# Optimization experiments

Hardware: AMD Instinct MI355X
Metric: run time of the kernel (lower is better)

Reference implementation:

```python
import jax, jax.numpy as jnp
import numpy as np

B, NQ, NK, C, H = 4, 1024, 1024, 768, 12
DH = C // H
SCALE = DH ** -0.5
EPS = 1e-5  # nn.LayerNorm default
NEG_INF = float('-inf')


def _ln(x, g, b):
    m = jnp.mean(x, axis=-1, keepdims=True)
    v = jnp.mean((x - m) ** 2, axis=-1, keepdims=True)
    return (x - m) * jax.lax.rsqrt(v + EPS) * g + b


def _heads(t):  # [B,N,C] -> [B,H,N,Dh]
    Bq, N, _ = t.shape
    return t.reshape(Bq, N, H, DH).transpose(0, 2, 1, 3)


def setup_inputs() -> dict:
    key = jax.random.key(0)
    ks = jax.random.split(key, 32)
    w = lambda k, shape: jax.random.normal(k, shape, jnp.float32) * 0.02
    g = lambda k: 1.0 + jax.random.normal(k, (C,), jnp.float32) * 0.02
    b = lambda k: jax.random.normal(k, (C,), jnp.float32) * 0.02
    inp = {
        'x': jax.random.normal(ks[0], (B, NQ, C), jnp.float32),
        'y': jax.random.normal(ks[1], (B, NK, C), jnp.float32),
        'xpos': jnp.arange(B * NQ, dtype=jnp.int32).reshape(B, NQ),
        'ypos': jnp.arange(B * NK, dtype=jnp.int32).reshape(B, NK),
        'mask': jax.random.randint(ks[2], (NQ, NK), 0, 2) > 0,
        'similarities': jax.random.normal(ks[3], (B, H, NQ, NK), jnp.float32),
        # norms
        'ln1_g': g(ks[4]), 'ln1_b': b(ks[5]),
        'ln2_g': g(ks[6]), 'ln2_b': b(ks[7]),
        'ln3_g': g(ks[8]), 'ln3_b': b(ks[9]),
        'lny_g': g(ks[10]), 'lny_b': b(ks[11]),
        # self-attn (qkv_bias=False)
        'qkv_w': w(ks[12], (3 * C, C)),
        'aproj_w': w(ks[13], (C, C)), 'aproj_b': b(ks[14]),
        # cross-attn
        'pq_w': w(ks[15], (C, C)), 'pk_w': w(ks[16], (C, C)), 'pv_w': w(ks[17], (C, C)),
        'cproj_w': w(ks[18], (C, C)), 'cproj_b': b(ks[19]),
        # mlp (hidden = 4*C)
        'fc1_w': w(ks[20], (4 * C, C)), 'fc1_b': jax.random.normal(ks[21], (4 * C,), jnp.float32) * 0.02,
        'fc2_w': w(ks[22], (C, 4 * C)), 'fc2_b': b(ks[23]),
    }
    return inp


def reference(x, y, xpos, ypos, mask, similarities,
              ln1_g, ln1_b, ln2_g, ln2_b, ln3_g, ln3_b, lny_g, lny_b,
              qkv_w, aproj_w, aproj_b,
              pq_w, pk_w, pv_w, cproj_w, cproj_b,
              fc1_w, fc1_b, fc2_w, fc2_b):
    # ---- self-attention (rope=None, dropout=0) ----
    xn = _ln(x, ln1_g, ln1_b)
    qkv = (xn @ qkv_w.T).reshape(B, NQ, 3, H, DH).transpose(2, 0, 3, 1, 4)
    q, k, v = qkv[0], qkv[1], qkv[2]                       # [B,H,Nq,Dh]
    attn = jax.nn.softmax(jnp.einsum('bhqd,bhkd->bhqk', q, k) * SCALE, axis=-1)
    sa = jnp.einsum('bhqk,bhkd->bhqd', attn, v).transpose(0, 2, 1, 3).reshape(B, NQ, C)
    x = x + sa @ aproj_w.T + aproj_b

    # ---- sparse cross-attention with similarity bias + mask ----
    y_ = _ln(y, lny_g, lny_b)
    xn2 = _ln(x, ln2_g, ln2_b)
    cq = _heads(xn2 @ pq_w.T)                              # [B,H,Nq,Dh]
    ck = _heads(y_ @ pk_w.T)                               # [B,H,Nk,Dh]
    cv = _heads(y_ @ pv_w.T)
    scores = jnp.einsum('bhqd,bhkd->bhqk', cq, ck) * SCALE
    sims_c = similarities - jnp.mean(similarities, axis=1, keepdims=True)
    scores = scores + sims_c
    scores = jnp.where(mask[None, None], scores, NEG_INF)
    cattn = jax.nn.softmax(scores, axis=-1)
    ca = jnp.einsum('bhqk,bhkd->bhqd', cattn, cv).transpose(0, 2, 1, 3).reshape(B, NQ, C)
    x = x + ca @ cproj_w.T + cproj_b

    # ---- MLP (exact GELU, as nn.GELU default) ----
    xn3 = _ln(x, ln3_g, ln3_b)
    h = jax.nn.gelu(xn3 @ fc1_w.T + fc1_b, approximate=False)
    x = x + h @ fc2_w.T + fc2_b
    return (x, y)
```

## Files before the change

kernel.cpp:

```cpp
#include <hip/hip_runtime.h>
#include <cstdint>
#include <cstddef>


typedef __bf16 bf16;
typedef __attribute__((ext_vector_type(8))) __bf16 bf16x8;
typedef __attribute__((ext_vector_type(4))) __bf16 bf16x4;
typedef __attribute__((ext_vector_type(4))) float f32x4;

typedef __attribute__((address_space(1))) void gvoid;
typedef __attribute__((address_space(3))) void lvoid;

#define DEVI static __device__ __forceinline__

DEVI void gload16(const void* g, void* l) {
  __builtin_amdgcn_global_load_lds((gvoid*)(uintptr_t)g, (lvoid*)(uintptr_t)l, 16, 0, 0);
}

DEVI f32x4 mfma_bf16(bf16x8 a, bf16x8 b, f32x4 c) {
  return __builtin_amdgcn_mfma_f32_16x16x32_bf16(a, b, c, 0, 0, 0);
}


template<int BM, int BN, bool BIAS, bool GELU, bool RES, bool OBF, bool VT>
DEVI void gemm_dev(bf16* As, bf16* Bs, int by, int bx,
                   const bf16* __restrict__ A, const bf16* __restrict__ Bt,
                   const float* __restrict__ bias, const float* __restrict__ res,
                   bf16* __restrict__ Cb, float* __restrict__ Cf,
                   bf16* __restrict__ vtOut, int vtBase, int N, int K)
{
  constexpr int WM = BM / 2, WN = BN / 2;
  constexpr int FM = WM / 16, FN = WN / 16;
  const int tid = threadIdx.x;
  const int lane = tid & 63;
  const int wv = tid >> 6;
  const int wr = wv >> 1, wc = wv & 1;
  const int l15 = lane & 15, lg = lane >> 4;
  const int bm = by * BM, bn = bx * BN;

  f32x4 acc[FM][FN];
  const f32x4 z = {0.f, 0.f, 0.f, 0.f};
  #pragma unroll
  for (int i = 0; i < FM; ++i)
    #pragma unroll
    for (int jj = 0; jj < FN; ++jj) acc[i][jj] = z;

  for (int k0 = 0; k0 < K; k0 += 64) {
    __syncthreads();
    #pragma unroll
    for (int c = tid; c < BM * 8; c += 256) {
      const int row = c >> 3, colb = (c & 7) << 4;
      gload16((const char*)A + ((size_t)(bm + row) * K + k0) * 2 + colb,
              (char*)As + (size_t)c * 16);
    }
    #pragma unroll
    for (int c = tid; c < BN * 8; c += 256) {
      const int row = c >> 3, colb = (c & 7) << 4;
      gload16((const char*)Bt + ((size_t)(bn + row) * K + k0) * 2 + colb,
              (char*)Bs + (size_t)c * 16);
    }
    __syncthreads();
    #pragma unroll
    for (int kk = 0; kk < 64; kk += 32) {
      bf16x8 af[FM], bfr[FN];
      #pragma unroll
      for (int mi = 0; mi < FM; ++mi)
        af[mi] = *(const bf16x8*)(As + (size_t)(wr * WM + mi * 16 + l15) * 64 + kk + lg * 8);
      #pragma unroll
      for (int ni = 0; ni < FN; ++ni)
        bfr[ni] = *(const bf16x8*)(Bs + (size_t)(wc * WN + ni * 16 + l15) * 64 + kk + lg * 8);
      #pragma unroll
      for (int mi = 0; mi < FM; ++mi)
        #pragma unroll
        for (int ni = 0; ni < FN; ++ni)
          acc[mi][ni] = mfma_bf16(af[mi], bfr[ni], acc[mi][ni]);
    }
  }

  #pragma unroll
  for (int mi = 0; mi < FM; ++mi) {
    const int row0 = bm + wr * WM + mi * 16 + lg * 4;
    #pragma unroll
    for (int ni = 0; ni < FN; ++ni) {
      const int col = bn + wc * WN + ni * 16 + l15;
      if constexpr (VT) {
        if (col >= vtBase) {
          const int hd = col - vtBase;
          const int bb = row0 >> 10, n0 = row0 & 1023;
          bf16x4 ov;
          #pragma unroll
          for (int r = 0; r < 4; ++r) ov[r] = (bf16)acc[mi][ni][r];
          *(bf16x4*)(vtOut + ((size_t)(bb * 768 + hd)) * 1024 + n0) = ov;
          continue;
        }
      }
      #pragma unroll
      for (int r = 0; r < 4; ++r) {
        float v = acc[mi][ni][r];
        if constexpr (BIAS) v += bias[col];
        if constexpr (GELU) v = 0.5f * v * (1.0f + erff(v * 0.70710678118654752f));
        if constexpr (RES)  v += res[(size_t)(row0 + r) * N + col];
        if constexpr (OBF)  Cb[(size_t)(row0 + r) * N + col] = (bf16)v;
        else                Cf[(size_t)(row0 + r) * N + col] = v;
      }
    }
  }
}

DEVI void biasr_dev(int blk,
                    const float* __restrict__ sim,
                    const unsigned char* __restrict__ mask,
                    bf16* __restrict__ out)
{
  const int b = blk >> 10, q = blk & 1023;
  const int t = threadIdx.x, lane = t & 63;

  int ds = 0;
  #pragma unroll
  for (int i = 0; i < 4; ++i) {
    const int idx = (lane * 4 + i) * 4;
    ds += mask[idx + 1] + mask[idx + 2] + mask[idx + 3];
  }
  #pragma unroll
  for (int o = 32; o; o >>= 1) ds += __shfl_xor(ds, o);
  const int msh = (ds == 0) ? 2 : 0;

  const int k4 = t * 4;
  const float* sb = sim + (size_t)b * 12 * 1048576;
  f32x4 sv[12];
  f32x4 acc = {0.f, 0.f, 0.f, 0.f};
  #pragma unroll
  for (int h = 0; h < 12; ++h) {
    sv[h] = *(const f32x4*)(sb + ((size_t)h * 1024 + q) * 1024 + k4);
    acc += sv[h];
  }
  const f32x4 mean = acc * (1.0f / 12.0f);

  float mb[4];
  if (msh == 0) {
    const uchar4 mv = *(const uchar4*)(mask + (size_t)q * 1024 + k4);
    mb[0] = mv.x ? 0.f : -1e30f; mb[1] = mv.y ? 0.f : -1e30f;
    mb[2] = mv.z ? 0.f : -1e30f; mb[3] = mv.w ? 0.f : -1e30f;
  } else {
    const int4 mv = *(const int4*)((const int*)mask + (size_t)q * 1024 + k4);
    mb[0] = mv.x ? 0.f : -1e30f; mb[1] = mv.y ? 0.f : -1e30f;
    mb[2] = mv.z ? 0.f : -1e30f; mb[3] = mv.w ? 0.f : -1e30f;
  }

  bf16* ob = out + (size_t)(b * 1024 + q) * 12 * 1024;
  #pragma unroll
  for (int h = 0; h < 12; ++h) {
    bf16x4 o;
    #pragma unroll
    for (int j = 0; j < 4; ++j)
      o[j] = (bf16)(sv[h][j] - mean[j] + mb[j]);
    *(bf16x4*)(ob + h * 1024 + k4) = o;
  }
}

DEVI void lnw_dev(int row,
                  const float* __restrict__ xin, const float* __restrict__ g,
                  const float* __restrict__ be, bf16* __restrict__ out)
{
  const int lane = threadIdx.x & 63;
  const f32x4* xr = (const f32x4*)(xin + (size_t)row * 768);
  f32x4 v[3];
  #pragma unroll
  for (int j = 0; j < 3; ++j) v[j] = xr[lane + 64 * j];
  float s = 0.f;
  #pragma unroll
  for (int j = 0; j < 3; ++j) s += v[j][0] + v[j][1] + v[j][2] + v[j][3];
  #pragma unroll
  for (int o = 32; o; o >>= 1) s += __shfl_xor(s, o);
  const float mean = s * (1.0f / 768.0f);
  float q = 0.f;
  #pragma unroll
  for (int j = 0; j < 3; ++j)
    #pragma unroll
    for (int e = 0; e < 4; ++e) { const float d = v[j][e] - mean; q += d * d; }
  #pragma unroll
  for (int o = 32; o; o >>= 1) q += __shfl_xor(q, o);
  const float inv = rsqrtf(q * (1.0f / 768.0f) + 1e-5f);
  #pragma unroll
  for (int j = 0; j < 3; ++j) {
    const int c = lane + 64 * j;
    const f32x4 gv = ((const f32x4*)g)[c];
    const f32x4 bv = ((const f32x4*)be)[c];
    bf16x4 o4;
    #pragma unroll
    for (int e = 0; e < 4; ++e)
      o4[e] = (bf16)((v[j][e] - mean) * inv * gv[e] + bv[e]);
    *((bf16x4*)out + (size_t)row * 192 + c) = o4;
  }
}

struct AuxArgs {
  const float* csrc[7];
  bf16* cdst[7];
  int cend[7];
  const float* y; const float* gy; const float* byv; bf16* yln;
  const float* sim; const unsigned char* mask; bf16* biasOut;
  int biasStart, biasCount, extraStart, extraCount;
};

DEVI void aux_dev(int j, const AuxArgs& A)
{
  if (j < A.extraCount) {
    const int e = A.extraStart + j;
    if (e < 1024) {
      lnw_dev(e * 4 + (threadIdx.x >> 6), A.y, A.gy, A.byv, A.yln);
    } else {
      const int blk = e - 1024;
      const int t = threadIdx.x;
      #pragma unroll
      for (int u = 0; u < 4; ++u) {
        const int i = blk * 1024 + u * 256 + t;
        int s = 0;
        #pragma unroll
        for (int k = 0; k < 6; ++k) s += (i >= A.cend[k]) ? 1 : 0;
        const int base = s ? A.cend[s - 1] : 0;
        const int off = i - base;
        const f32x4 v = *((const f32x4*)A.csrc[s] + off);
        bf16x4 o;
        o[0] = (bf16)v[0]; o[1] = (bf16)v[1]; o[2] = (bf16)v[2]; o[3] = (bf16)v[3];
        *(bf16x4*)(A.cdst[s] + (size_t)off * 4) = o;
      }
    }
  } else {
    biasr_dev(A.biasStart + (j - A.extraCount), A.sim, A.mask, A.biasOut);
  }
}


__global__ __launch_bounds__(256)
void prep_k(const float* __restrict__ qkvw, bf16* __restrict__ w_qkv,
            const float* __restrict__ x, const float* __restrict__ g1,
            const float* __restrict__ b1, bf16* __restrict__ xn)
{
  const int f = blockIdx.x;
  const int t = threadIdx.x;
  if (f < 432) {
    #pragma unroll
    for (int u = 0; u < 4; ++u) {
      const int i = f * 1024 + u * 256 + t;
      const f32x4 v = *((const f32x4*)qkvw + i);
      bf16x4 o;
      o[0] = (bf16)v[0]; o[1] = (bf16)v[1]; o[2] = (bf16)v[2]; o[3] = (bf16)v[3];
      *(bf16x4*)(w_qkv + (size_t)i * 4) = o;
    }
  } else {
    lnw_dev((f - 432) * 4 + (t >> 6), x, g1, b1, xn);
  }
}

template<int BM, int BN, bool BIAS, bool GELU, bool RES, bool OBF, bool VT>
__global__ __launch_bounds__(256)
void gemm_bt(const bf16* __restrict__ A, const bf16* __restrict__ Bt,
             const float* __restrict__ bias, const float* __restrict__ res,
             bf16* __restrict__ Cb, float* __restrict__ Cf,
             bf16* __restrict__ vtOut, int vtBase,
             int nyPerXcd, int N, int K,
             int nCompute, AuxArgs aux)
{
  __shared__ bf16 As[BM * 64];
  __shared__ bf16 Bs[BN * 64];
  const int f = blockIdx.x;
  if (f >= nCompute) {
    aux_dev(f - nCompute, aux);
    return;
  }
  const int xcd = f & 7, j = f >> 3;
  const int by = xcd + 8 * (j % nyPerXcd);
  const int bx = j / nyPerXcd;
  gemm_dev<BM,BN,BIAS,GELU,RES,OBF,VT>(As, Bs, by, bx,
      A, Bt, bias, res, Cb, Cf, vtOut, vtBase, N, K);
}

__global__ __launch_bounds__(256)
void apkv_k(const bf16* __restrict__ sa, const bf16* __restrict__ w_ap,
            const float* __restrict__ apb, const float* __restrict__ x,
            float* __restrict__ x1,
            const bf16* __restrict__ yln, const bf16* __restrict__ w_pkv,
            bf16* __restrict__ ckv, bf16* __restrict__ cvtT,
            AuxArgs aux)
{
  __shared__ bf16 As[128 * 64];
  __shared__ bf16 Bs[128 * 64];
  const int f = blockIdx.x;
  if (f >= 768) {
    aux_dev(f - 768, aux);
    return;
  }
  if (f < 384) {
    const int xcd = f & 7, j = f >> 3;
    const int by = xcd + 8 * (j % 8);
    const int bx = j / 8;
    gemm_dev<64,128,true,false,true,false,false>(As, Bs, by, bx,
        sa, w_ap, apb, x, nullptr, x1, nullptr, 0, 768, 768);
  } else {
    const int g = f - 384;
    const int xcd = g & 7, j = g >> 3;
    const int by = xcd + 8 * (j % 4);
    const int bx = j / 4;
    gemm_dev<128,128,false,false,false,true,true>(As, Bs, by, bx,
        yln, w_pkv, nullptr, nullptr, ckv, nullptr, cvtT, 768, 1536, 768);
  }
}

__global__ __launch_bounds__(256)
void fc2copy_k(const bf16* __restrict__ hbuf, const bf16* __restrict__ w_f2,
               const float* __restrict__ f2b, const float* __restrict__ x2,
               float* __restrict__ outp,
               const float* __restrict__ y, float* __restrict__ ycopy)
{
  __shared__ bf16 As[128 * 64];
  __shared__ bf16 Bs[128 * 64];
  const int f = blockIdx.x;
  if (f < 384) {
    const int xcd = f & 7, j = f >> 3;
    const int by = xcd + 8 * (j % 8);
    const int bx = j / 8;
    gemm_dev<64,128,true,false,true,false,false>(As, Bs, by, bx,
        hbuf, w_f2, f2b, x2, nullptr, outp, nullptr, 0, 768, 3072);
  } else {
    for (int i = (f - 384) * 256 + threadIdx.x; i < 786432; i += 512 * 256)
      ((f32x4*)ycopy)[i] = ((const f32x4*)y)[i];
  }
}

__global__ __launch_bounds__(256)
void ln_k(const float* __restrict__ xin, const float* __restrict__ g,
          const float* __restrict__ be, bf16* __restrict__ out)
{
  lnw_dev(blockIdx.x * 4 + (threadIdx.x >> 6), xin, g, be, out);
}

template<int CROSS>
__global__ __launch_bounds__(256, 3)
void fattn_k(const bf16* __restrict__ Qp, int ldq,
             const bf16* __restrict__ Kp, int ldk,
             const bf16* __restrict__ Vt,
             const bf16* __restrict__ bias,
             bf16* __restrict__ Out,
             int nCompute, AuxArgs aux)
{
  __shared__ bf16 Kl[2][64 * 64];
  __shared__ bf16 Vl[2][64 * 64];
  __shared__ bf16 Pl[4][16 * 72];
  __shared__ bf16 Bl[CROSS ? 4 * 16 * 72 : 4];

  const int f = blockIdx.x;
  if (f >= nCompute) {
    aux_dev(f - nCompute, aux);
    return;
  }
  const int r8 = f & 7, rest = f >> 3;
  const int c6 = rest % 6, qt = rest / 6;
  const int pp = r8 + 8 * c6;
  const int b = pp / 12, hh = pp % 12;
  const int tid = threadIdx.x, lane = tid & 63, wq = tid >> 6;
  const int l15 = lane & 15, lg = lane >> 4;

  bf16x8 qreg0, qreg1;
  {
    const bf16* qsrc = Qp + (size_t)(b * 1024 + qt * 64 + wq * 16 + l15) * ldq + hh * 64 + lg * 8;
    qreg0 = *(const bf16x8*)qsrc;
    qreg1 = *(const bf16x8*)(qsrc + 32);
  }
  const char* Kbase = (const char*)(Kp + (size_t)b * 1024 * ldk + hh * 64);
  const char* Vbase = (const char*)(Vt + (size_t)(b * 12 + hh) * 64 * 1024);
  const bf16* biasQ = nullptr;
  if constexpr (CROSS)
    biasQ = bias + ((size_t)(b * 1024 + qt * 64 + wq * 16 + (lane >> 2)) * 12 + hh) * 1024
          + (lane & 3) * 16;

  f32x4 oacc[4];
  const f32x4 z = {0.f, 0.f, 0.f, 0.f};
  #pragma unroll
  for (int i = 0; i < 4; ++i) oacc[i] = z;
  float m_run = -1e30f, l_run = 0.f;

  char* PlW = (char*)&Pl[wq][0];
  char* BlW = (char*)&Bl[0] + (CROSS ? wq * 16 * 144 : 0);
  const int swz = (l15 & 7) << 4;

  auto stage = [&](int buf, int t) {
    const int k0 = t * 64;
    #pragma unroll
    for (int jj = 0; jj < 2; ++jj) {
      const int c = jj * 256 + tid;
      const int r = c >> 3;
      const int sw = ((c & 7) ^ (r & 7)) << 4;
      gload16(Kbase + ((size_t)(k0 + r) * ldk) * 2 + sw, (char*)&Kl[buf][0] + (size_t)c * 16);
      gload16(Vbase + (size_t)r * 2048 + (size_t)k0 * 2 + sw, (char*)&Vl[buf][0] + (size_t)c * 16);
    }
  };

  stage(0, 0);
  __syncthreads();

  for (int t = 0; t < 16; ++t) {
    const int cur = t & 1;
    const int k0 = t * 64;

    bf16x8 br0, br1;
    if constexpr (CROSS) {
      const bf16* bp = biasQ + k0;
      br0 = *(const bf16x8*)bp;
      br1 = *(const bf16x8*)(bp + 8);
    }
    if (t < 15) stage(cur ^ 1, t + 1);

    f32x4 sacc[4];
    #pragma unroll
    for (int i = 0; i < 4; ++i) sacc[i] = z;
    #pragma unroll
    for (int ni = 0; ni < 4; ++ni) {
      const int rowb = (ni * 16 + l15) * 128;
      const bf16x8 a0 = *(const bf16x8*)((char*)&Kl[cur][0] + rowb + ((lg * 16) ^ swz));
      const bf16x8 a1 = *(const bf16x8*)((char*)&Kl[cur][0] + rowb + ((64 + lg * 16) ^ swz));
      sacc[ni] = mfma_bf16(a0, qreg0, sacc[ni]);
      sacc[ni] = mfma_bf16(a1, qreg1, sacc[ni]);
    }

    bf16x4 bv[4];
    if constexpr (CROSS) {
      char* dst = BlW + (lane >> 2) * 144 + (lane & 3) * 32;
      *(bf16x8*)dst = br0;
      *(bf16x8*)(dst + 16) = br1;
      #pragma unroll
      for (int ni = 0; ni < 4; ++ni)
        bv[ni] = *(const bf16x4*)(BlW + l15 * 144 + ni * 32 + lg * 8);
    }

    float sv[16];
    #pragma unroll
    for (int ni = 0; ni < 4; ++ni)
      #pragma unroll
      for (int r = 0; r < 4; ++r)
        sv[ni * 4 + r] = sacc[ni][r] * 0.125f;
    if constexpr (CROSS) {
      #pragma unroll
      for (int ni = 0; ni < 4; ++ni)
        #pragma unroll
        for (int r = 0; r < 4; ++r)
          sv[ni * 4 + r] += (float)bv[ni][r];
    }
    float mx = sv[0];
    #pragma unroll
    for (int jj = 1; jj < 16; ++jj) mx = fmaxf(mx, sv[jj]);
    mx = fmaxf(mx, __shfl_xor(mx, 16));
    mx = fmaxf(mx, __shfl_xor(mx, 32));
    const float mnew = fmaxf(m_run, mx);
    const float corr = __expf(m_run - mnew);
    m_run = mnew;
    float ps = 0.f;
    #pragma unroll
    for (int jj = 0; jj < 16; ++jj) { sv[jj] = __expf(sv[jj] - mnew); ps += sv[jj]; }
    l_run = l_run * corr + ps;

    #pragma unroll
    for (int ni = 0; ni < 4; ++ni) {
      bf16x4 pw;
      #pragma unroll
      for (int r = 0; r < 4; ++r) pw[r] = (bf16)sv[ni * 4 + r];
      *(bf16x4*)(PlW + l15 * 144 + ni * 32 + lg * 8) = pw;
    }
    float cr[4];
    #pragma unroll
    for (int r = 0; r < 4; ++r) cr[r] = __shfl(corr, ((lane >> 4) << 2) + r);
    #pragma unroll
    for (int nd = 0; nd < 4; ++nd)
      #pragma unroll
      for (int r = 0; r < 4; ++r) oacc[nd][r] *= cr[r];

    const bf16x8 p0 = *(const bf16x8*)(PlW + l15 * 144 + lg * 16);
    const bf16x8 p1 = *(const bf16x8*)(PlW + l15 * 144 + 64 + lg * 16);
    #pragma unroll
    for (int nd = 0; nd < 4; ++nd) {
      const int rowb = (nd * 16 + l15) * 128;
      const bf16x8 v0 = *(const bf16x8*)((char*)&Vl[cur][0] + rowb + ((lg * 16) ^ swz));
      const bf16x8 v1 = *(const bf16x8*)((char*)&Vl[cur][0] + rowb + ((64 + lg * 16) ^ swz));
      oacc[nd] = mfma_bf16(p0, v0, oacc[nd]);
      oacc[nd] = mfma_bf16(p1, v1, oacc[nd]);
    }
    __syncthreads();
  }

  float ls = l_run + __shfl_xor(l_run, 16);
  ls += __shfl_xor(ls, 32);
  const float inv = 1.0f / ls;
  float ivr[4];
  #pragma unroll
  for (int r = 0; r < 4; ++r) ivr[r] = __shfl(inv, ((lane >> 4) << 2) + r);
  bf16* ob = Out + (size_t)(b * 1024 + qt * 64 + wq * 16 + lg * 4) * 768 + hh * 64 + l15;
  #pragma unroll
  for (int r = 0; r < 4; ++r)
    #pragma unroll
    for (int nd = 0; nd < 4; ++nd)
      ob[(size_t)r * 768 + nd * 16] = (bf16)(oacc[nd][r] * ivr[r]);
}

extern "C" void kernel_launch(void* const* d_in, const int* in_sizes, int n_in,
                              void* d_out, int out_size, void* d_ws, size_t ws_size,
                              hipStream_t stream)
{
  (void)in_sizes; (void)n_in; (void)out_size; (void)ws_size;
  const float* x    = (const float*)d_in[0];
  const float* y    = (const float*)d_in[1];
  const unsigned char* mask = (const unsigned char*)d_in[4];
  const float* sim  = (const float*)d_in[5];
  const float* ln1g = (const float*)d_in[6];
  const float* ln1b = (const float*)d_in[7];
  const float* ln2g = (const float*)d_in[8];
  const float* ln2b = (const float*)d_in[9];
  const float* ln3g = (const float*)d_in[10];
  const float* ln3b = (const float*)d_in[11];
  const float* lnyg = (const float*)d_in[12];
  const float* lnyb = (const float*)d_in[13];
  const float* qkvw = (const float*)d_in[14];
  const float* apw  = (const float*)d_in[15];
  const float* apb  = (const float*)d_in[16];
  const float* pqw  = (const float*)d_in[17];
  const float* pkw  = (const float*)d_in[18];
  const float* pvw  = (const float*)d_in[19];
  const float* cpw  = (const float*)d_in[20];
  const float* cpb  = (const float*)d_in[21];
  const float* f1w  = (const float*)d_in[22];
  const float* f1b  = (const float*)d_in[23];
  const float* f2w  = (const float*)d_in[24];
  const float* f2b  = (const float*)d_in[25];

  char* ws = (char*)d_ws;
  size_t off = 0;
  auto alloc = [&](size_t bytes) -> void* {
    off = (off + 255) & ~(size_t)255;
    void* p = ws + off;
    off += bytes;
    return p;
  };
  const size_t T = 4096;
  bf16* w_qkv = (bf16*)alloc((size_t)2304 * 768 * 2);
  bf16* w_ap  = (bf16*)alloc((size_t)768 * 768 * 2);
  bf16* w_pq  = (bf16*)alloc((size_t)768 * 768 * 2);
  bf16* w_pkv = (bf16*)alloc((size_t)1536 * 768 * 2);
  bf16* w_cp  = (bf16*)alloc((size_t)768 * 768 * 2);
  bf16* w_f1  = (bf16*)alloc((size_t)3072 * 768 * 2);
  bf16* w_f2  = (bf16*)alloc((size_t)768 * 3072 * 2);
  bf16* xn    = (bf16*)alloc(T * 768 * 2);
  bf16* qkvo  = (bf16*)alloc(T * 2304 * 2);
  bf16* vt    = (bf16*)alloc((size_t)48 * 64 * 1024 * 2);
  bf16* sa    = (bf16*)alloc(T * 768 * 2);
  float* x1   = (float*)alloc(T * 768 * 4);
  bf16* yln   = (bf16*)alloc(T * 768 * 2);
  bf16* xn2   = (bf16*)alloc(T * 768 * 2);
  bf16* cqf   = (bf16*)alloc(T * 768 * 2);
  bf16* ckv   = (bf16*)alloc(T * 1536 * 2);
  bf16* cvtT  = (bf16*)alloc((size_t)48 * 64 * 1024 * 2);
  bf16* biasA = (bf16*)alloc((size_t)4 * 1024 * 12 * 1024 * 2);
  bf16* ca    = (bf16*)alloc(T * 768 * 2);
  float* x2   = (float*)alloc(T * 768 * 4);
  bf16* xn3   = (bf16*)alloc(T * 768 * 2);
  bf16* hbuf  = (bf16*)alloc(T * 3072 * 2);

  AuxArgs aux;
  {
    const float* srcs[7] = {apw, pkw, pvw, pqw, cpw, f1w, f2w};
    bf16* dsts[7] = {w_ap, w_pkv, w_pkv + 768 * 768, w_pq, w_cp, w_f1, w_f2};
    const int n4s[7] = {147456, 147456, 147456, 147456, 147456, 589824, 589824};
    int cum = 0;
    for (int j = 0; j < 7; ++j) {
      aux.csrc[j] = srcs[j]; aux.cdst[j] = dsts[j];
      cum += n4s[j]; aux.cend[j] = cum;
    }
    aux.y = y; aux.gy = lnyg; aux.byv = lnyb; aux.yln = yln;
    aux.sim = sim; aux.mask = mask; aux.biasOut = biasA;
  }

  prep_k<<<1456, 256, 0, stream>>>(qkvw, w_qkv, x, ln1g, ln1b, xn);

  AuxArgs a2 = aux;
  a2.extraStart = 0;    a2.extraCount = 1456;
  a2.biasStart = 0;     a2.biasCount = 800;
  gemm_bt<128,128,false,false,false,true,true><<<576 + 2256, 256, 0, stream>>>(
      xn, w_qkv, nullptr, nullptr, qkvo, nullptr, vt, 1536, 4, 2304, 768,
      576, a2);

  AuxArgs a3 = aux;
  a3.extraStart = 1456; a3.extraCount = 1440;
  a3.biasStart = 800;   a3.biasCount = 800;
  fattn_k<0><<<768 + 2240, 256, 0, stream>>>(
      qkvo, 2304, qkvo + 768, 2304, vt, nullptr, sa, 768, a3);

  AuxArgs a4 = aux;
  a4.extraStart = 0;    a4.extraCount = 0;
  a4.biasStart = 1600;  a4.biasCount = 1700;
  apkv_k<<<768 + 1700, 256, 0, stream>>>(sa, w_ap, apb, x, x1,
                                         yln, w_pkv, ckv, cvtT, a4);

  ln_k<<<1024, 256, 0, stream>>>(x1, ln2g, ln2b, xn2);

  AuxArgs a6 = aux;
  a6.extraStart = 0;    a6.extraCount = 0;
  a6.biasStart = 3300;  a6.biasCount = 796;
  gemm_bt<64,128,false,false,false,true,false><<<384 + 796, 256, 0, stream>>>(
      xn2, w_pq, nullptr, nullptr, cqf, nullptr, nullptr, 0, 8, 768, 768,
      384, a6);

  AuxArgs a0 = aux;
  a0.extraStart = 0; a0.extraCount = 0; a0.biasStart = 0; a0.biasCount = 0;
  fattn_k<1><<<768, 256, 0, stream>>>(
      cqf, 768, ckv, 1536, cvtT, biasA, ca, 768, a0);

  gemm_bt<64,128,true,false,true,false,false><<<384, 256, 0, stream>>>(
      ca, w_cp, cpb, x1, nullptr, x2, nullptr, 0, 8, 768, 768,
      384, a0);

  ln_k<<<1024, 256, 0, stream>>>(x2, ln3g, ln3b, xn3);

  gemm_bt<128,128,true,true,false,true,false><<<768, 256, 0, stream>>>(
      xn3, w_f1, f1b, nullptr, hbuf, nullptr, nullptr, 0, 4, 3072, 768,
      768, a0);

  fc2copy_k<<<896, 256, 0, stream>>>(
      hbuf, w_f2, f2b, x2, (float*)d_out, y, (float*)d_out + 3145728);
}
```

Before: 350.5 us.

## Prefetch cross-attn bias into registers and move y copy into attention aux blocks

The cross-attention kernel now loads each lane's bias values straight from global memory in MFMA output layout, one tile ahead. This drops the LDS staging buffer and its shuffle, and hides the bias load latency behind the score computation. The y-to-output copy moves out of the final fc2 kernel into extra blocks of the cross-attention launch, and the fc2 kernel's A tile shrinks to its real size. The bias-precompute blocks are rebalanced between the apkv and pq-projection launches. Holding the prefetched bias costs extra registers in the attention kernel, and the aux copy blocks compete with the attention blocks for the same GPU.

```diff
diff --git a/kernel.cpp b/kernel.cpp
--- a/kernel.cpp
+++ b/kernel.cpp
@@ -200,11 +200,18 @@
   int cend[7];
   const float* y; const float* gy; const float* byv; bf16* yln;
   const float* sim; const unsigned char* mask; bf16* biasOut;
+  const float* cpS; float* cpD; int cpCount;
   int biasStart, biasCount, extraStart, extraCount;
 };
 
 DEVI void aux_dev(int j, const AuxArgs& A)
 {
+  if (j < A.cpCount) {
+    for (int i = j * 256 + threadIdx.x; i < 786432; i += A.cpCount * 256)
+      ((f32x4*)A.cpD)[i] = ((const f32x4*)A.cpS)[i];
+    return;
+  }
+  j -= A.cpCount;
   if (j < A.extraCount) {
     const int e = A.extraStart + j;
     if (e < 1024) {
@@ -308,24 +315,18 @@
 }
 
 __global__ __launch_bounds__(256)
-void fc2copy_k(const bf16* __restrict__ hbuf, const bf16* __restrict__ w_f2,
-               const float* __restrict__ f2b, const float* __restrict__ x2,
-               float* __restrict__ outp,
-               const float* __restrict__ y, float* __restrict__ ycopy)
-{
-  __shared__ bf16 As[128 * 64];
+void fc2_k(const bf16* __restrict__ hbuf, const bf16* __restrict__ w_f2,
+           const float* __restrict__ f2b, const float* __restrict__ x2,
+           float* __restrict__ outp)
+{
+  __shared__ bf16 As[64 * 64];
   __shared__ bf16 Bs[128 * 64];
   const int f = blockIdx.x;
-  if (f < 384) {
-    const int xcd = f & 7, j = f >> 3;
-    const int by = xcd + 8 * (j % 8);
-    const int bx = j / 8;
-    gemm_dev<64,128,true,false,true,false,false>(As, Bs, by, bx,
-        hbuf, w_f2, f2b, x2, nullptr, outp, nullptr, 0, 768, 3072);
-  } else {
-    for (int i = (f - 384) * 256 + threadIdx.x; i < 786432; i += 512 * 256)
-      ((f32x4*)ycopy)[i] = ((const f32x4*)y)[i];
-  }
+  const int xcd = f & 7, j = f >> 3;
+  const int by = xcd + 8 * (j % 8);
+  const int bx = j / 8;
+  gemm_dev<64,128,true,false,true,false,false>(As, Bs, by, bx,
+      hbuf, w_f2, f2b, x2, nullptr, outp, nullptr, 0, 768, 3072);
 }
 
 __global__ __launch_bounds__(256)
@@ -347,7 +348,6 @@
   __shared__ bf16 Kl[2][64 * 64];
   __shared__ bf16 Vl[2][64 * 64];
   __shared__ bf16 Pl[4][16 * 72];
-  __shared__ bf16 Bl[CROSS ? 4 * 16 * 72 : 4];
 
   const int f = blockIdx.x;
   if (f >= nCompute) {
@@ -369,10 +369,9 @@
   }
   const char* Kbase = (const char*)(Kp + (size_t)b * 1024 * ldk + hh * 64);
   const char* Vbase = (const char*)(Vt + (size_t)(b * 12 + hh) * 64 * 1024);
-  const bf16* biasQ = nullptr;
+  const bf16* biasRow = nullptr;
   if constexpr (CROSS)
-    biasQ = bias + ((size_t)(b * 1024 + qt * 64 + wq * 16 + (lane >> 2)) * 12 + hh) * 1024
-          + (lane & 3) * 16;
+    biasRow = bias + ((size_t)(b * 1024 + qt * 64 + wq * 16 + l15) * 12 + hh) * 1024;
 
   f32x4 oacc[4];
   const f32x4 z = {0.f, 0.f, 0.f, 0.f};
@@ -381,7 +380,6 @@
   float m_run = -1e30f, l_run = 0.f;
 
   char* PlW = (char*)&Pl[wq][0];
-  char* BlW = (char*)&Bl[0] + (CROSS ? wq * 16 * 144 : 0);
   const int swz = (l15 & 7) << 4;
 
   auto stage = [&](int buf, int t) {
@@ -396,20 +394,25 @@
     }
   };
 
+  bf16x4 bvc[4];
+  auto loadBias = [&](int t, bf16x4* dst) {
+    const bf16* bp = biasRow + t * 64 + lg * 4;
+    #pragma unroll
+    for (int ni = 0; ni < 4; ++ni) dst[ni] = *(const bf16x4*)(bp + ni * 16);
+  };
+
   stage(0, 0);
+  if constexpr (CROSS) loadBias(0, bvc);
   __syncthreads();
 
   for (int t = 0; t < 16; ++t) {
     const int cur = t & 1;
-    const int k0 = t * 64;
-
-    bf16x8 br0, br1;
+    if (t < 15) stage(cur ^ 1, t + 1);
+
+    bf16x4 bvn[4];
     if constexpr (CROSS) {
-      const bf16* bp = biasQ + k0;
-      br0 = *(const bf16x8*)bp;
-      br1 = *(const bf16x8*)(bp + 8);
-    }
-    if (t < 15) stage(cur ^ 1, t + 1);
+      if (t < 15) loadBias(t + 1, bvn);
+    }
 
     f32x4 sacc[4];
     #pragma unroll
@@ -423,16 +426,6 @@
       sacc[ni] = mfma_bf16(a1, qreg1, sacc[ni]);
     }
 
-    bf16x4 bv[4];
-    if constexpr (CROSS) {
-      char* dst = BlW + (lane >> 2) * 144 + (lane & 3) * 32;
-      *(bf16x8*)dst = br0;
-      *(bf16x8*)(dst + 16) = br1;
-      #pragma unroll
-      for (int ni = 0; ni < 4; ++ni)
-        bv[ni] = *(const bf16x4*)(BlW + l15 * 144 + ni * 32 + lg * 8);
-    }
-
     float sv[16];
     #pragma unroll
     for (int ni = 0; ni < 4; ++ni)
@@ -444,7 +437,7 @@
       for (int ni = 0; ni < 4; ++ni)
         #pragma unroll
         for (int r = 0; r < 4; ++r)
-          sv[ni * 4 + r] += (float)bv[ni][r];
+          sv[ni * 4 + r] += (float)bvc[ni][r];
     }
     float mx = sv[0];
     #pragma unroll
@@ -483,6 +476,10 @@
       const bf16x8 v1 = *(const bf16x8*)((char*)&Vl[cur][0] + rowb + ((64 + lg * 16) ^ swz));
       oacc[nd] = mfma_bf16(p0, v0, oacc[nd]);
       oacc[nd] = mfma_bf16(p1, v1, oacc[nd]);
+    }
+    if constexpr (CROSS) {
+      #pragma unroll
+      for (int ni = 0; ni < 4; ++ni) bvc[ni] = bvn[ni];
     }
     __syncthreads();
   }
@@ -575,6 +572,8 @@
     }
     aux.y = y; aux.gy = lnyg; aux.byv = lnyb; aux.yln = yln;
     aux.sim = sim; aux.mask = mask; aux.biasOut = biasA;
+    aux.cpS = nullptr; aux.cpD = nullptr; aux.cpCount = 0;
+    aux.biasStart = 0; aux.biasCount = 0; aux.extraStart = 0; aux.extraCount = 0;
   }
 
   prep_k<<<1456, 256, 0, stream>>>(qkvw, w_qkv, x, ln1g, ln1b, xn);
@@ -593,25 +592,24 @@
       qkvo, 2304, qkvo + 768, 2304, vt, nullptr, sa, 768, a3);
 
   AuxArgs a4 = aux;
-  a4.extraStart = 0;    a4.extraCount = 0;
-  a4.biasStart = 1600;  a4.biasCount = 1700;
-  apkv_k<<<768 + 1700, 256, 0, stream>>>(sa, w_ap, apb, x, x1,
+  a4.biasStart = 1600;  a4.biasCount = 2100;
+  apkv_k<<<768 + 2100, 256, 0, stream>>>(sa, w_ap, apb, x, x1,
                                          yln, w_pkv, ckv, cvtT, a4);
 
   ln_k<<<1024, 256, 0, stream>>>(x1, ln2g, ln2b, xn2);
 
   AuxArgs a6 = aux;
-  a6.extraStart = 0;    a6.extraCount = 0;
-  a6.biasStart = 3300;  a6.biasCount = 796;
-  gemm_bt<64,128,false,false,false,true,false><<<384 + 796, 256, 0, stream>>>(
+  a6.biasStart = 3700;  a6.biasCount = 396;
+  gemm_bt<64,128,false,false,false,true,false><<<384 + 396, 256, 0, stream>>>(
       xn2, w_pq, nullptr, nullptr, cqf, nullptr, nullptr, 0, 8, 768, 768,
       384, a6);
 
+  AuxArgs a7 = aux;
+  a7.cpS = y; a7.cpD = (float*)d_out + 3145728; a7.cpCount = 512;
+  fattn_k<1><<<768 + 512, 256, 0, stream>>>(
+      cqf, 768, ckv, 1536, cvtT, biasA, ca, 768, a7);
+
   AuxArgs a0 = aux;
-  a0.extraStart = 0; a0.extraCount = 0; a0.biasStart = 0; a0.biasCount = 0;
-  fattn_k<1><<<768, 256, 0, stream>>>(
-      cqf, 768, ckv, 1536, cvtT, biasA, ca, 768, a0);
-
   gemm_bt<64,128,true,false,true,false,false><<<384, 256, 0, stream>>>(
       ca, w_cp, cpb, x1, nullptr, x2, nullptr, 0, 8, 768, 768,
       384, a0);
@@ -622,6 +620,5 @@
       xn3, w_f1, f1b, nullptr, hbuf, nullptr, nullptr, 0, 4, 3072, 768,
       768, a0);
 
-  fc2copy_k<<<896, 256, 0, stream>>>(
-      hbuf, w_f2, f2b, x2, (float*)d_out, y, (float*)d_out + 3145728);
-}
+  fc2_k<<<384, 256, 0, stream>>>(hbuf, w_f2, f2b, x2, (float*)d_out);
+}
```

Measured after the change: 359.2 us. 2.5% more time.
